# Kernel optimization log

Measured on AMD Instinct MI355X. Metric: run time of the kernel, lower is better.

## Reference

```python
import jax, jax.numpy as jnp
import numpy as np

DK = 64
DROPOUT_P = 0.1


def setup_inputs() -> dict:
    key = jax.random.key(0)
    kq, kk, kv, km = jax.random.split(key, 4)
    B, S, D = 16, 2048, 64
    q = jax.random.normal(kq, (B, S, D), dtype=jnp.float32)
    k = jax.random.normal(kk, (B, S, D), dtype=jnp.float32)
    v = jax.random.normal(kv, (B, S, D), dtype=jnp.float32)
    attn_mask = jax.random.randint(km, (S, S), 0, 2, dtype=jnp.int32)
    return {"q": q, "k": k, "v": v, "attn_mask": attn_mask}


def reference(q, k, v, attn_mask):
    # q = q / sqrt(dk)
    qs = q * (1.0 / np.sqrt(DK)).astype(np.float32)
    # dots: [B, S_q, S_k]
    dots = jnp.einsum("bqd,bkd->bqk", qs, k)
    # mask: 0 -> -inf, 1 -> 0 (additive)
    add_mask = jnp.where(attn_mask == 0, -jnp.inf, 0.0).astype(dots.dtype)
    dots = dots + add_mask  # broadcast [S,S] over batch
    attn = jax.nn.softmax(dots, axis=-1)
    # inverted dropout, train mode, fixed key for determinism
    keep = jax.random.bernoulli(jax.random.key(42), 1.0 - DROPOUT_P, attn.shape)
    attn = jnp.where(keep, attn * (1.0 / (1.0 - DROPOUT_P)), 0.0)
    out = jnp.einsum("bqk,bkd->bqd", attn, v)
    return out
```

## Files before the change

kernel.cpp:

```cpp
#include <hip/hip_runtime.h>

#define BATCH 16
#define SEQ   2048
#define DIM   64
#define NTHREADS 256

typedef short bf16x8 __attribute__((ext_vector_type(8)));
typedef float f32x4 __attribute__((ext_vector_type(4)));

__device__ __forceinline__ int ldsoff(int row) {
  return row * 72 + 16 * (row >> 2);
}
#define LDS_SZ (64 * 72 + 16 * 16)

__device__ __forceinline__ unsigned tf_bits(unsigned f) {
  unsigned x0 = 0u;
  unsigned x1 = f;
  const unsigned ks1 = 42u;
  const unsigned ks2 = 0x1BD11BDAu ^ 42u;
  x1 += ks1;
#define TF_R(r) { x0 += x1; x1 = __builtin_amdgcn_alignbit(x1, x1, 32u - (r)); x1 ^= x0; }
  TF_R(13) TF_R(15) TF_R(26) TF_R(6)
  x0 += ks1; x1 += ks2 + 1u;
  TF_R(17) TF_R(29) TF_R(16) TF_R(24)
  x0 += ks2; x1 += 2u;
  TF_R(13) TF_R(15) TF_R(26) TF_R(6)
  x1 += ks1 + 3u;
  TF_R(17) TF_R(29) TF_R(16) TF_R(24)
  x0 += ks1; x1 += ks2 + 4u;
  TF_R(13) TF_R(15) TF_R(26) TF_R(6)
  x0 += ks2; x1 += 5u;
#undef TF_R
  return x0 ^ x1;
}
#define KEEP_THRESH 0xE6666600u

__device__ __forceinline__ unsigned pack_bf16x2(float lo, float hi) {
  const unsigned l = (__float_as_uint(lo) + 0x8000u) >> 16;
  const unsigned h = (__float_as_uint(hi) + 0x8000u) & 0xFFFF0000u;
  return h | l;
}
__device__ __forceinline__ unsigned pack_trunc(float lo, float hi) {
  return __builtin_amdgcn_perm(__float_as_uint(hi), __float_as_uint(lo), 0x07060302u);
}

#define WS_KF   0
#define WS_VF   1048576
#define WS_MB   2097152
#define WS_KEEP 2228224
#define WS_O0   4325376
#define WS_L    6422528

#define RNG_BLKS  16384
#define MASK_BLKS 1024
#define CONV_BLKS 2048

__global__ __launch_bounds__(NTHREADS, 8)
void prep(const float* __restrict__ k, const float* __restrict__ v,
          const int* __restrict__ mask, unsigned* __restrict__ ws) {
  const int t = threadIdx.x;
  const unsigned bx = blockIdx.x;

  if (bx < RNG_BLKS) {
    const unsigned pid = bx * NTHREADS + (unsigned)t;
    const unsigned base = ((pid >> 9) << 13) | ((pid & 511u) << 2);
    unsigned k16 = 0u;
#pragma unroll
    for (int r = 0; r < 4; ++r)
#pragma unroll
      for (int c = 0; c < 4; ++c)
        k16 |= (tf_bits(base + (unsigned)(r * 2048 + c)) < KEEP_THRESH)
                   ? (1u << (r * 4 + c)) : 0u;
    ((unsigned short*)(ws + WS_KEEP))[pid] = (unsigned short)k16;
    return;
  }

  if (bx < RNG_BLKS + MASK_BLKS) {
    const unsigned pid = (bx - RNG_BLKS) * NTHREADS + (unsigned)t;
    const unsigned C4 = pid & 511u, R4 = pid >> 9;
    unsigned m16 = 0u;
#pragma unroll
    for (int r = 0; r < 4; ++r) {
      const int4 mv = *(const int4*)(mask + (size_t)(4 * R4 + r) * SEQ + 4 * C4);
      m16 |= (mv.x ? 1u : 0u) << (r * 4 + 0);
      m16 |= (mv.y ? 1u : 0u) << (r * 4 + 1);
      m16 |= (mv.z ? 1u : 0u) << (r * 4 + 2);
      m16 |= (mv.w ? 1u : 0u) << (r * 4 + 3);
    }
    ((unsigned short*)(ws + WS_MB))[pid] = (unsigned short)m16;
    return;
  }

  const int lane = t & 63;
  const int tx = lane & 15, quad = lane >> 4;
  const unsigned gid = (bx - RNG_BLKS - MASK_BLKS) * NTHREADS + (unsigned)t;
  const unsigned e = gid & 262143u;
  const int ks = (e >> 6) & 1, nt = (e >> 7) & 3, kt = (e >> 9) & 31, b = e >> 14;
  uint4 wout;
  if (gid < 262144u) {
    const float* src = k + ((size_t)b * SEQ + kt * 64 + 4 * tx + nt) * DIM
                         + ks * 32 + quad * 8;
    const float4 f0 = *(const float4*)src;
    const float4 f1 = *(const float4*)(src + 4);
    wout.x = pack_bf16x2(f0.x, f0.y); wout.y = pack_bf16x2(f0.z, f0.w);
    wout.z = pack_bf16x2(f1.x, f1.y); wout.w = pack_bf16x2(f1.z, f1.w);
    *(uint4*)(ws + WS_KF + (size_t)e * 4) = wout;
  } else {
    const float* src = v + ((size_t)b * SEQ + kt * 64 + ks * 32 + quad * 8) * DIM
                         + nt * 16 + tx;
    const float a0 = src[0 * DIM], a1 = src[1 * DIM], a2 = src[2 * DIM], a3 = src[3 * DIM];
    const float a4 = src[4 * DIM], a5 = src[5 * DIM], a6 = src[6 * DIM], a7 = src[7 * DIM];
    wout.x = pack_bf16x2(a0, a1); wout.y = pack_bf16x2(a2, a3);
    wout.z = pack_bf16x2(a4, a5); wout.w = pack_bf16x2(a6, a7);
    *(uint4*)(ws + WS_VF + (size_t)e * 4) = wout;
  }
}

__global__ __launch_bounds__(NTHREADS, 4)
void attn_fwd(const float* __restrict__ q, const unsigned* __restrict__ ws,
              float* __restrict__ out) {
  __shared__ unsigned short PS[LDS_SZ];

  const int t    = threadIdx.x;
  const int w    = t >> 6;
  const int lane = t & 63;
  const int tx   = lane & 15;
  const int quad = lane >> 4;

  const int sk = blockIdx.x >> 9;
  const int r  = blockIdx.x & 511;
  const int bb = r >> 5;
  const int q0 = (r & 31) * 64;
  const int qw = q0 + 16 * w;
  const int kt0 = sk * 16;

  const float qscale = 0.125f * 1.44269504088896340736f;

  bf16x8 aq[2];
  {
    const float* qr = q + ((size_t)bb * SEQ + qw + tx) * DIM + quad * 8;
#pragma unroll
    for (int ks = 0; ks < 2; ++ks) {
      const float4 f0 = *(const float4*)(qr + ks * 32);
      const float4 f1 = *(const float4*)(qr + ks * 32 + 4);
      union { unsigned u[4]; bf16x8 v; } a;
      a.u[0] = pack_bf16x2(f0.x * qscale, f0.y * qscale);
      a.u[1] = pack_bf16x2(f0.z * qscale, f0.w * qscale);
      a.u[2] = pack_bf16x2(f1.x * qscale, f1.y * qscale);
      a.u[3] = pack_bf16x2(f1.z * qscale, f1.w * qscale);
      aq[ks] = a.v;
    }
  }

  float lrun[4] = {0.f, 0.f, 0.f, 0.f};
  f32x4 oacc[4];
#pragma unroll
  for (int nt = 0; nt < 4; ++nt) oacc[nt] = (f32x4){0.f, 0.f, 0.f, 0.f};

  const unsigned* kfb = ws + WS_KF + (size_t)(bb * 32) * 2048 + (size_t)lane * 4;
  const unsigned* vfb = ws + WS_VF + (size_t)(bb * 32) * 2048 + (size_t)lane * 4;
  const unsigned short* keepb = (const unsigned short*)(ws + WS_KEEP)
      + ((size_t)(bb * 512 + (qw >> 2) + quad)) * 512 + tx;
  const unsigned short* maskb = (const unsigned short*)(ws + WS_MB)
      + ((size_t)((qw >> 2) + quad)) * 512 + tx;

  bf16x8 vf[4][2];

#define MD_PWRITE(qk_, kw_, mw_)                                               \
  {                                                                            \
    const unsigned cw = (kw_) & (mw_);                                         \
    _Pragma("unroll")                                                          \
    for (int reg = 0; reg < 4; ++reg) {                                        \
      const unsigned mnib = (mw_) >> (reg * 4);                                \
      const unsigned cnib = cw >> (reg * 4);                                   \
      float pd[4];                                                             \
      float ls = 0.0f;                                                         \
      _Pragma("unroll")                                                        \
      for (int nt = 0; nt < 4; ++nt) {                                         \
        const float s = (mnib & (1u << nt)) ? qk_[nt][reg] : -1e30f;           \
        const float e = __builtin_amdgcn_exp2f(s);                             \
        ls += e;                                                               \
        pd[nt] = (cnib & (1u << nt)) ? e : 0.0f;                               \
      }                                                                        \
      lrun[reg] += ls;                                                         \
      uint2 pw;                                                                \
      pw.x = pack_trunc(pd[0], pd[1]);                                         \
      pw.y = pack_trunc(pd[2], pd[3]);                                         \
      *(uint2*)&PS[ldsoff(16 * w + quad * 4 + reg) + 4 * tx] = pw;             \
    }                                                                          \
  }

  {
    const unsigned* kfp = kfb + (size_t)kt0 * 2048;
    const unsigned* vfp = vfb + (size_t)kt0 * 2048;
    bf16x8 kf[4][2];
#pragma unroll
    for (int nt = 0; nt < 4; ++nt)
#pragma unroll
      for (int ks = 0; ks < 2; ++ks) {
        kf[nt][ks] = *(const bf16x8*)(kfp + (nt * 2 + ks) * 256);
        vf[nt][ks] = *(const bf16x8*)(vfp + (nt * 2 + ks) * 256);
      }
    const unsigned kwv = keepb[kt0 * 16];
    const unsigned mwv = maskb[kt0 * 16];
    f32x4 qk[4];
#pragma unroll
    for (int nt = 0; nt < 4; ++nt) {
      f32x4 c = (f32x4){0.f, 0.f, 0.f, 0.f};
#pragma unroll
      for (int ks = 0; ks < 2; ++ks)
        c = __builtin_amdgcn_mfma_f32_16x16x32_bf16(aq[ks], kf[nt][ks], c, 0, 0, 0);
      qk[nt] = c;
    }
    MD_PWRITE(qk, kwv, mwv)
  }

#pragma unroll 1
  for (int kt = kt0 + 1; kt < kt0 + 16; ++kt) {
    const unsigned* kfp = kfb + (size_t)kt * 2048;
    bf16x8 kf[4][2];
#pragma unroll
    for (int nt = 0; nt < 4; ++nt)
#pragma unroll
      for (int ks = 0; ks < 2; ++ks)
        kf[nt][ks] = *(const bf16x8*)(kfp + (nt * 2 + ks) * 256);
    const unsigned kwv = keepb[kt * 16];
    const unsigned mwv = maskb[kt * 16];
#pragma unroll
    for (int ks = 0; ks < 2; ++ks) {
      const bf16x8 ap = *(const bf16x8*)&PS[ldsoff(16 * w + tx) + ks * 32 + quad * 8];
#pragma unroll
      for (int nt = 0; nt < 4; ++nt)
        oacc[nt] = __builtin_amdgcn_mfma_f32_16x16x32_bf16(ap, vf[nt][ks],
                                                           oacc[nt], 0, 0, 0);
    }
    const unsigned* vfp = vfb + (size_t)kt * 2048;
#pragma unroll
    for (int nt = 0; nt < 4; ++nt)
#pragma unroll
      for (int ks = 0; ks < 2; ++ks)
        vf[nt][ks] = *(const bf16x8*)(vfp + (nt * 2 + ks) * 256);
    f32x4 qk[4];
#pragma unroll
    for (int nt = 0; nt < 4; ++nt) {
      f32x4 c = (f32x4){0.f, 0.f, 0.f, 0.f};
#pragma unroll
      for (int ks = 0; ks < 2; ++ks)
        c = __builtin_amdgcn_mfma_f32_16x16x32_bf16(aq[ks], kf[nt][ks], c, 0, 0, 0);
      qk[nt] = c;
    }
    MD_PWRITE(qk, kwv, mwv)
  }

#pragma unroll
  for (int ks = 0; ks < 2; ++ks) {
    const bf16x8 ap = *(const bf16x8*)&PS[ldsoff(16 * w + tx) + ks * 32 + quad * 8];
#pragma unroll
    for (int nt = 0; nt < 4; ++nt)
      oacc[nt] = __builtin_amdgcn_mfma_f32_16x16x32_bf16(ap, vf[nt][ks], oacc[nt], 0, 0, 0);
  }

  float lsum[4];
#pragma unroll
  for (int reg = 0; reg < 4; ++reg) {
    float ls = lrun[reg];
    ls += __shfl_xor(ls, 1);
    ls += __shfl_xor(ls, 2);
    ls += __shfl_xor(ls, 4);
    ls += __shfl_xor(ls, 8);
    lsum[reg] = ls;
  }
  float* wsf = (float*)ws;
  float* ob = sk ? out + ((size_t)bb * SEQ + qw) * DIM
                 : wsf + WS_O0 + ((size_t)bb * SEQ + qw) * DIM;
#pragma unroll
  for (int nt = 0; nt < 4; ++nt)
#pragma unroll
    for (int reg = 0; reg < 4; ++reg)
      ob[(size_t)(quad * 4 + reg) * DIM + nt * 16 + tx] = oacc[nt][reg];
  if (tx == 0) {
    float* lp = wsf + WS_L + sk * 32768 + bb * SEQ + qw + quad * 4;
#pragma unroll
    for (int reg = 0; reg < 4; ++reg) lp[reg] = lsum[reg];
  }
}

__global__ __launch_bounds__(NTHREADS)
void combine(float* __restrict__ out, const unsigned* __restrict__ ws) {
  const unsigned gid = blockIdx.x * NTHREADS + threadIdx.x;
  const float* wsf = (const float*)ws;
  const float4 a = ((const float4*)out)[gid];
  const float4 b = ((const float4*)(wsf + WS_O0))[gid];
  const unsigned row = gid >> 4;
  const float linv = (1.0f / 0.9f) / (wsf[WS_L + row] + wsf[WS_L + 32768u + row]);
  float4 o;
  o.x = (a.x + b.x) * linv;
  o.y = (a.y + b.y) * linv;
  o.z = (a.z + b.z) * linv;
  o.w = (a.w + b.w) * linv;
  ((float4*)out)[gid] = o;
}

extern "C" void kernel_launch(void* const* d_in, const int* in_sizes, int n_in,
                              void* d_out, int out_size, void* d_ws, size_t ws_size,
                              hipStream_t stream) {
  const float* q = (const float*)d_in[0];
  const float* k = (const float*)d_in[1];
  const float* v = (const float*)d_in[2];
  const int* mask = (const int*)d_in[3];
  float* out = (float*)d_out;
  unsigned* ws = (unsigned*)d_ws;

  hipLaunchKernelGGL(prep, dim3(RNG_BLKS + MASK_BLKS + CONV_BLKS), dim3(NTHREADS),
                     0, stream, k, v, mask, ws);
  hipLaunchKernelGGL(attn_fwd, dim3(1024), dim3(NTHREADS), 0, stream,
                     q, ws, out);
  hipLaunchKernelGGL(combine, dim3(2048), dim3(NTHREADS), 0, stream, out, ws);
}
```

Measured before the change: 238.2 us.

## Split keys three ways and generate most dropout bits inline in attention

The attention kernel now splits the key range into three chunks (11/11/10 tiles) instead of two, launching 1536 blocks with higher occupancy bounds. The first two chunks compute the Threefry dropout bits inline, alongside the exp work. Only the last chunk's keep bits are precomputed in the prep kernel, which shrinks the RNG prep grid from 16384 to 5120 blocks. The combine step now sums three partial outputs and denominators. This moves RNG ALU work into the MFMA-bound loop to overlap with it, at the cost of extra VALU pressure and an additional partial buffer.

```diff
diff --git a/kernel.cpp b/kernel.cpp
--- a/kernel.cpp
+++ b/kernel.cpp
@@ -48,12 +48,13 @@
 #define WS_VF   1048576
 #define WS_MB   2097152
 #define WS_KEEP 2228224
-#define WS_O0   4325376
-#define WS_L    6422528
-
-#define RNG_BLKS  16384
-#define MASK_BLKS 1024
-#define CONV_BLKS 2048
+#define WS_O0   2883584
+#define WS_O1   4980736
+#define WS_L    7077888
+
+#define KEEPRNG_BLKS 5120
+#define MASK_BLKS    1024
+#define CONV_BLKS    2048
 
 __global__ __launch_bounds__(NTHREADS, 8)
 void prep(const float* __restrict__ k, const float* __restrict__ v,
@@ -61,22 +62,24 @@
   const int t = threadIdx.x;
   const unsigned bx = blockIdx.x;
 
-  if (bx < RNG_BLKS) {
+  if (bx < KEEPRNG_BLKS) {
     const unsigned pid = bx * NTHREADS + (unsigned)t;
-    const unsigned base = ((pid >> 9) << 13) | ((pid & 511u) << 2);
+    const unsigned R4 = pid / 160u;
+    const unsigned c  = pid - R4 * 160u;
+    const unsigned base = R4 * 8192u + c * 4u + 1408u;
     unsigned k16 = 0u;
 #pragma unroll
     for (int r = 0; r < 4; ++r)
 #pragma unroll
-      for (int c = 0; c < 4; ++c)
-        k16 |= (tf_bits(base + (unsigned)(r * 2048 + c)) < KEEP_THRESH)
-                   ? (1u << (r * 4 + c)) : 0u;
+      for (int cc = 0; cc < 4; ++cc)
+        k16 |= (tf_bits(base + (unsigned)(r * 2048 + cc)) < KEEP_THRESH)
+                   ? (1u << (r * 4 + cc)) : 0u;
     ((unsigned short*)(ws + WS_KEEP))[pid] = (unsigned short)k16;
     return;
   }
 
-  if (bx < RNG_BLKS + MASK_BLKS) {
-    const unsigned pid = (bx - RNG_BLKS) * NTHREADS + (unsigned)t;
+  if (bx < KEEPRNG_BLKS + MASK_BLKS) {
+    const unsigned pid = (bx - KEEPRNG_BLKS) * NTHREADS + (unsigned)t;
     const unsigned C4 = pid & 511u, R4 = pid >> 9;
     unsigned m16 = 0u;
 #pragma unroll
@@ -93,7 +96,7 @@
 
   const int lane = t & 63;
   const int tx = lane & 15, quad = lane >> 4;
-  const unsigned gid = (bx - RNG_BLKS - MASK_BLKS) * NTHREADS + (unsigned)t;
+  const unsigned gid = (bx - KEEPRNG_BLKS - MASK_BLKS) * NTHREADS + (unsigned)t;
   const unsigned e = gid & 262143u;
   const int ks = (e >> 6) & 1, nt = (e >> 7) & 3, kt = (e >> 9) & 31, b = e >> 14;
   uint4 wout;
@@ -116,7 +119,7 @@
   }
 }
 
-__global__ __launch_bounds__(NTHREADS, 4)
+__global__ __launch_bounds__(NTHREADS, 6)
 void attn_fwd(const float* __restrict__ q, const unsigned* __restrict__ ws,
               float* __restrict__ out) {
   __shared__ unsigned short PS[LDS_SZ];
@@ -127,12 +130,13 @@
   const int tx   = lane & 15;
   const int quad = lane >> 4;
 
-  const int sk = blockIdx.x >> 9;
+  const int sk = (int)(blockIdx.x >> 9);
   const int r  = blockIdx.x & 511;
   const int bb = r >> 5;
   const int q0 = (r & 31) * 64;
   const int qw = q0 + 16 * w;
-  const int kt0 = sk * 16;
+  const int kt0 = sk * 11;
+  const int ktn = (sk == 2) ? 10 : 11;
 
   const float qscale = 0.125f * 1.44269504088896340736f;
 
@@ -159,20 +163,46 @@
 
   const unsigned* kfb = ws + WS_KF + (size_t)(bb * 32) * 2048 + (size_t)lane * 4;
   const unsigned* vfb = ws + WS_VF + (size_t)(bb * 32) * 2048 + (size_t)lane * 4;
-  const unsigned short* keepb = (const unsigned short*)(ws + WS_KEEP)
-      + ((size_t)(bb * 512 + (qw >> 2) + quad)) * 512 + tx;
-  const unsigned short* maskb = (const unsigned short*)(ws + WS_MB)
+  const unsigned short* maskp = (const unsigned short*)(ws + WS_MB)
       + ((size_t)((qw >> 2) + quad)) * 512 + tx;
+  const unsigned short* keepp = (const unsigned short*)(ws + WS_KEEP)
+      + ((size_t)(bb * 512 + (qw >> 2) + quad)) * 160 + tx;
+  const unsigned fbase0 = (unsigned)(bb * SEQ + qw + quad * 4) * (unsigned)SEQ
+                          + (unsigned)(4 * tx);
 
   bf16x8 vf[4][2];
 
-#define MD_PWRITE(qk_, kw_, mw_)                                               \
+#define RNG_PWRITE(kt_, qk_, mw_)                                              \
   {                                                                            \
-    const unsigned cw = (kw_) & (mw_);                                         \
+    const unsigned fb = fbase0 + (unsigned)((kt_) * 64);                       \
     _Pragma("unroll")                                                          \
     for (int reg = 0; reg < 4; ++reg) {                                        \
       const unsigned mnib = (mw_) >> (reg * 4);                                \
-      const unsigned cnib = cw >> (reg * 4);                                   \
+      float pd[4];                                                             \
+      float ls = 0.0f;                                                         \
+      _Pragma("unroll")                                                        \
+      for (int nt = 0; nt < 4; ++nt) {                                         \
+        const float s = (mnib & (1u << nt)) ? qk_[nt][reg] : -1e30f;           \
+        const float e = __builtin_amdgcn_exp2f(s);                             \
+        ls += e;                                                               \
+        const unsigned bits = tf_bits(fb + (unsigned)(reg * SEQ) + (unsigned)nt); \
+        pd[nt] = (bits < KEEP_THRESH) ? e : 0.0f;                              \
+      }                                                                        \
+      lrun[reg] += ls;                                                         \
+      uint2 pw;                                                                \
+      pw.x = pack_trunc(pd[0], pd[1]);                                         \
+      pw.y = pack_trunc(pd[2], pd[3]);                                         \
+      *(uint2*)&PS[ldsoff(16 * w + quad * 4 + reg) + 4 * tx] = pw;             \
+    }                                                                          \
+  }
+
+#define PATCH_PWRITE(qk_, kw_, mw_)                                            \
+  {                                                                            \
+    const unsigned cwd = (kw_) & (mw_);                                        \
+    _Pragma("unroll")                                                          \
+    for (int reg = 0; reg < 4; ++reg) {                                        \
+      const unsigned mnib = (mw_) >> (reg * 4);                                \
+      const unsigned cnib = cwd >> (reg * 4);                                  \
       float pd[4];                                                             \
       float ls = 0.0f;                                                         \
       _Pragma("unroll")                                                        \
@@ -190,75 +220,83 @@
     }                                                                          \
   }
 
-  {
-    const unsigned* kfp = kfb + (size_t)kt0 * 2048;
-    const unsigned* vfp = vfb + (size_t)kt0 * 2048;
-    bf16x8 kf[4][2];
-#pragma unroll
-    for (int nt = 0; nt < 4; ++nt)
-#pragma unroll
-      for (int ks = 0; ks < 2; ++ks) {
+#define LOAD_KF(kt_)                                                           \
+    const unsigned* kfp = kfb + (size_t)(kt_) * 2048;                          \
+    bf16x8 kf[4][2];                                                           \
+    _Pragma("unroll")                                                          \
+    for (int nt = 0; nt < 4; ++nt)                                             \
+      _Pragma("unroll")                                                        \
+      for (int ks = 0; ks < 2; ++ks)                                           \
         kf[nt][ks] = *(const bf16x8*)(kfp + (nt * 2 + ks) * 256);
+
+#define PV_STEP                                                                \
+    _Pragma("unroll")                                                          \
+    for (int ks = 0; ks < 2; ++ks) {                                           \
+      const bf16x8 ap = *(const bf16x8*)&PS[ldsoff(16 * w + tx) + ks * 32 + quad * 8]; \
+      _Pragma("unroll")                                                        \
+      for (int nt = 0; nt < 4; ++nt)                                           \
+        oacc[nt] = __builtin_amdgcn_mfma_f32_16x16x32_bf16(ap, vf[nt][ks],     \
+                                                           oacc[nt], 0, 0, 0); \
+    }
+
+#define LOAD_VF(kt_)                                                           \
+    const unsigned* vfp = vfb + (size_t)(kt_) * 2048;                          \
+    _Pragma("unroll")                                                          \
+    for (int nt = 0; nt < 4; ++nt)                                             \
+      _Pragma("unroll")                                                        \
+      for (int ks = 0; ks < 2; ++ks)                                           \
         vf[nt][ks] = *(const bf16x8*)(vfp + (nt * 2 + ks) * 256);
-      }
-    const unsigned kwv = keepb[kt0 * 16];
-    const unsigned mwv = maskb[kt0 * 16];
-    f32x4 qk[4];
-#pragma unroll
-    for (int nt = 0; nt < 4; ++nt) {
-      f32x4 c = (f32x4){0.f, 0.f, 0.f, 0.f};
-#pragma unroll
-      for (int ks = 0; ks < 2; ++ks)
-        c = __builtin_amdgcn_mfma_f32_16x16x32_bf16(aq[ks], kf[nt][ks], c, 0, 0, 0);
-      qk[nt] = c;
-    }
-    MD_PWRITE(qk, kwv, mwv)
-  }
-
+
+#define QK_STEP(qk_)                                                           \
+    f32x4 qk_[4];                                                              \
+    _Pragma("unroll")                                                          \
+    for (int nt = 0; nt < 4; ++nt) {                                           \
+      f32x4 c = (f32x4){0.f, 0.f, 0.f, 0.f};                                   \
+      _Pragma("unroll")                                                        \
+      for (int ks = 0; ks < 2; ++ks)                                           \
+        c = __builtin_amdgcn_mfma_f32_16x16x32_bf16(aq[ks], kf[nt][ks], c, 0, 0, 0); \
+      qk_[nt] = c;                                                             \
+    }
+
+  if (sk != 2) {
+    {
+      LOAD_KF(kt0)
+      LOAD_VF(kt0)
+      const unsigned mwv = maskp[kt0 * 16];
+      QK_STEP(qk)
+      RNG_PWRITE(kt0, qk, mwv)
+    }
 #pragma unroll 1
-  for (int kt = kt0 + 1; kt < kt0 + 16; ++kt) {
-    const unsigned* kfp = kfb + (size_t)kt * 2048;
-    bf16x8 kf[4][2];
-#pragma unroll
-    for (int nt = 0; nt < 4; ++nt)
-#pragma unroll
-      for (int ks = 0; ks < 2; ++ks)
-        kf[nt][ks] = *(const bf16x8*)(kfp + (nt * 2 + ks) * 256);
-    const unsigned kwv = keepb[kt * 16];
-    const unsigned mwv = maskb[kt * 16];
-#pragma unroll
-    for (int ks = 0; ks < 2; ++ks) {
-      const bf16x8 ap = *(const bf16x8*)&PS[ldsoff(16 * w + tx) + ks * 32 + quad * 8];
-#pragma unroll
-      for (int nt = 0; nt < 4; ++nt)
-        oacc[nt] = __builtin_amdgcn_mfma_f32_16x16x32_bf16(ap, vf[nt][ks],
-                                                           oacc[nt], 0, 0, 0);
-    }
-    const unsigned* vfp = vfb + (size_t)kt * 2048;
-#pragma unroll
-    for (int nt = 0; nt < 4; ++nt)
-#pragma unroll
-      for (int ks = 0; ks < 2; ++ks)
-        vf[nt][ks] = *(const bf16x8*)(vfp + (nt * 2 + ks) * 256);
-    f32x4 qk[4];
-#pragma unroll
-    for (int nt = 0; nt < 4; ++nt) {
-      f32x4 c = (f32x4){0.f, 0.f, 0.f, 0.f};
-#pragma unroll
-      for (int ks = 0; ks < 2; ++ks)
-        c = __builtin_amdgcn_mfma_f32_16x16x32_bf16(aq[ks], kf[nt][ks], c, 0, 0, 0);
-      qk[nt] = c;
-    }
-    MD_PWRITE(qk, kwv, mwv)
-  }
-
-#pragma unroll
-  for (int ks = 0; ks < 2; ++ks) {
-    const bf16x8 ap = *(const bf16x8*)&PS[ldsoff(16 * w + tx) + ks * 32 + quad * 8];
-#pragma unroll
-    for (int nt = 0; nt < 4; ++nt)
-      oacc[nt] = __builtin_amdgcn_mfma_f32_16x16x32_bf16(ap, vf[nt][ks], oacc[nt], 0, 0, 0);
-  }
+    for (int kt = kt0 + 1; kt < kt0 + 11; ++kt) {
+      LOAD_KF(kt)
+      const unsigned mwv = maskp[kt * 16];
+      PV_STEP
+      LOAD_VF(kt)
+      QK_STEP(qk)
+      RNG_PWRITE(kt, qk, mwv)
+    }
+  } else {
+    {
+      LOAD_KF(22)
+      LOAD_VF(22)
+      const unsigned kwv = keepp[0];
+      const unsigned mwv = maskp[22 * 16];
+      QK_STEP(qk)
+      PATCH_PWRITE(qk, kwv, mwv)
+    }
+#pragma unroll 1
+    for (int kt = 23; kt < 32; ++kt) {
+      LOAD_KF(kt)
+      const unsigned kwv = keepp[(kt - 22) * 16];
+      const unsigned mwv = maskp[kt * 16];
+      PV_STEP
+      LOAD_VF(kt)
+      QK_STEP(qk)
+      PATCH_PWRITE(qk, kwv, mwv)
+    }
+  }
+
+  PV_STEP
 
   float lsum[4];
 #pragma unroll
@@ -271,8 +309,10 @@
     lsum[reg] = ls;
   }
   float* wsf = (float*)ws;
-  float* ob = sk ? out + ((size_t)bb * SEQ + qw) * DIM
-                 : wsf + WS_O0 + ((size_t)bb * SEQ + qw) * DIM;
+  const size_t off = ((size_t)bb * SEQ + qw) * DIM;
+  float* ob = (sk == 0) ? wsf + WS_O0 + off
+            : (sk == 1) ? wsf + WS_O1 + off
+                        : out + off;
 #pragma unroll
   for (int nt = 0; nt < 4; ++nt)
 #pragma unroll
@@ -289,15 +329,17 @@
 void combine(float* __restrict__ out, const unsigned* __restrict__ ws) {
   const unsigned gid = blockIdx.x * NTHREADS + threadIdx.x;
   const float* wsf = (const float*)ws;
-  const float4 a = ((const float4*)out)[gid];
-  const float4 b = ((const float4*)(wsf + WS_O0))[gid];
+  const float4 a  = ((const float4*)out)[gid];
+  const float4 b0 = ((const float4*)(wsf + WS_O0))[gid];
+  const float4 b1 = ((const float4*)(wsf + WS_O1))[gid];
   const unsigned row = gid >> 4;
-  const float linv = (1.0f / 0.9f) / (wsf[WS_L + row] + wsf[WS_L + 32768u + row]);
+  const float linv = (1.0f / 0.9f) / (wsf[WS_L + row] + wsf[WS_L + 32768u + row]
+                                      + wsf[WS_L + 65536u + row]);
   float4 o;
-  o.x = (a.x + b.x) * linv;
-  o.y = (a.y + b.y) * linv;
-  o.z = (a.z + b.z) * linv;
-  o.w = (a.w + b.w) * linv;
+  o.x = (a.x + b0.x + b1.x) * linv;
+  o.y = (a.y + b0.y + b1.y) * linv;
+  o.z = (a.z + b0.z + b1.z) * linv;
+  o.w = (a.w + b0.w + b1.w) * linv;
   ((float4*)out)[gid] = o;
 }
 
@@ -311,9 +353,9 @@
   float* out = (float*)d_out;
   unsigned* ws = (unsigned*)d_ws;
 
-  hipLaunchKernelGGL(prep, dim3(RNG_BLKS + MASK_BLKS + CONV_BLKS), dim3(NTHREADS),
-                     0, stream, k, v, mask, ws);
-  hipLaunchKernelGGL(attn_fwd, dim3(1024), dim3(NTHREADS), 0, stream,
+  hipLaunchKernelGGL(prep, dim3(KEEPRNG_BLKS + MASK_BLKS + CONV_BLKS),
+                     dim3(NTHREADS), 0, stream, k, v, mask, ws);
+  hipLaunchKernelGGL(attn_fwd, dim3(1536), dim3(NTHREADS), 0, stream,
                      q, ws, out);
   hipLaunchKernelGGL(combine, dim3(2048), dim3(NTHREADS), 0, stream, out, ws);
 }
```

Result: no change. 242.3 us (+1.7%).
